# Kernel optimization log

Measured on AMD Instinct MI355X. Metric: run time of the kernel, lower is better.

Reference implementation:

```python
import jax, jax.numpy as jnp
import numpy as np

NOISE_WEIGHT = 1.0
CHAMFER_WEIGHT = 0.1
CHUNK = 1024


def _min_dist_chunked(a, b):
    """For each point in a [B,N,3], squared distance to nearest point in b [B,M,3].
    Processed in chunks of CHUNK points of `a` to avoid materializing [B,N,M].
    Returns [B,N]."""
    B, N, _ = a.shape
    b_sq = jnp.sum(b * b, axis=-1)  # [B,M]
    nc = N // CHUNK
    a_chunks = jnp.moveaxis(a.reshape(B, nc, CHUNK, 3), 1, 0)  # [nc,B,CHUNK,3]

    def body(carry, a_c):
        a_sq = jnp.sum(a_c * a_c, axis=-1)  # [B,CHUNK]
        # d[b,i,j] = |a_i|^2 + |b_j|^2 - 2 a_i.b_j
        d = a_sq[:, :, None] + b_sq[:, None, :] - 2.0 * jnp.einsum('bid,bjd->bij', a_c, b)
        d = jnp.maximum(d, 0.0)
        return carry, jnp.min(d, axis=2)  # [B,CHUNK]

    _, mins = jax.lax.scan(body, None, a_chunks)  # [nc,B,CHUNK]
    return jnp.moveaxis(mins, 0, 1).reshape(B, N)


def chamfer_distance(pred, target):
    d_pt = _min_dist_chunked(pred, target)   # [B,N]
    d_tp = _min_dist_chunked(target, pred)   # [B,M]
    return jnp.mean(d_pt, axis=1) + jnp.mean(d_tp, axis=1)  # [B]


def setup_inputs() -> dict:
    key = jax.random.key(0)
    k1, k2, k3, k4 = jax.random.split(key, 4)
    B, N = 8, 16384
    return {
        'predicted_noise': jax.random.normal(k1, (B, N, 3), dtype=jnp.float32),
        'actual_noise': jax.random.normal(k2, (B, N, 3), dtype=jnp.float32),
        'predicted_points_coarse': jax.random.normal(k3, (B, N, 3), dtype=jnp.float32),
        'target_points_coarse': jax.random.normal(k4, (B, N, 3), dtype=jnp.float32),
    }


def reference(predicted_noise, actual_noise, predicted_points_coarse, target_points_coarse):
    noise_loss = jnp.mean(jnp.abs(predicted_noise - actual_noise))
    chamfer_loss = jnp.mean(chamfer_distance(predicted_points_coarse, target_points_coarse))
    total_loss = NOISE_WEIGHT * noise_loss + CHAMFER_WEIGHT * chamfer_loss
    return total_loss
```

## Files before the change

### kernel.cpp

```cpp
#include <hip/hip_runtime.h>
#include <stdint.h>

#define NPTS        16384
#define BATCH       8
#define JC          512
#define NCHUNK      (NPTS / JC)
#define QPB         128
#define QBLKS       (NPTS / QPB)
#define CHAM_BLOCKS (BATCH * 2 * QBLKS)
#define NOISE_N     (BATCH * NPTS * 3)
#define NOISE_V4    (NOISE_N / 4)
#define NOISE_BLOCKS (NOISE_V4 / 256)
#define NPTS_TOT    (BATCH * NPTS)

#define WS_NOISE_PART 0
#define WS_CHAM_PART  4096
#define WS_PK_PRED    16384
#define WS_PK_TARG    (WS_PK_PRED + 8 * NPTS_TOT)
#define WS_R_PRED     (WS_PK_TARG + 8 * NPTS_TOT)
#define WS_R_TARG     (WS_R_PRED + 4 * NPTS_TOT)

using halfx8 = __attribute__((ext_vector_type(8))) _Float16;
using f32x16 = __attribute__((ext_vector_type(16))) float;

__device__ __forceinline__ unsigned short f2h(float f) {
  union { _Float16 h; unsigned short s; } v; v.h = (_Float16)f; return v.s;
}
__device__ __forceinline__ float h2f(unsigned short s) {
  union { _Float16 h; unsigned short u; } v; v.u = s; return (float)v.h;
}

__global__ void pack_kernel(const float* __restrict__ pred,
                            const float* __restrict__ targ,
                            ushort4* __restrict__ pk_pred,
                            ushort4* __restrict__ pk_targ,
                            float* __restrict__ r_pred,
                            float* __restrict__ r_targ) {
  int i = blockIdx.x * 256 + threadIdx.x;
  if (i >= NPTS_TOT) return;
  {
    float x = pred[3*i+0], y = pred[3*i+1], z = pred[3*i+2];
    float s = __builtin_fmaf(x, x, __builtin_fmaf(y, y, z*z));
    pk_pred[i] = make_ushort4(f2h(x), f2h(y), f2h(z), f2h(s));
    r_pred[i] = s;
  }
  {
    float x = targ[3*i+0], y = targ[3*i+1], z = targ[3*i+2];
    float s = __builtin_fmaf(x, x, __builtin_fmaf(y, y, z*z));
    pk_targ[i] = make_ushort4(f2h(x), f2h(y), f2h(z), f2h(s));
    r_targ[i] = s;
  }
}

__global__ void noise_kernel(const float4* __restrict__ a,
                             const float4* __restrict__ b,
                             float* __restrict__ part) {
  int i = blockIdx.x * 256 + threadIdx.x;
  float4 pa = a[i], pb = b[i];
  float s = fabsf(pa.x-pb.x) + fabsf(pa.y-pb.y) + fabsf(pa.z-pb.z) + fabsf(pa.w-pb.w);
  for (int o = 1; o < 64; o <<= 1) s += __shfl_xor(s, o);
  __shared__ float ws4[4];
  int lane = threadIdx.x & 63, wv = threadIdx.x >> 6;
  if (lane == 0) ws4[wv] = s;
  __syncthreads();
  if (threadIdx.x == 0) part[blockIdx.x] = ws4[0] + ws4[1] + ws4[2] + ws4[3];
}

__global__ __launch_bounds__(256, 4)
void chamfer_kernel(const ushort4* __restrict__ pk_pred,
                    const ushort4* __restrict__ pk_targ,
                    const float* __restrict__ r_pred,
                    const float* __restrict__ r_targ,
                    float* __restrict__ part) {
  __shared__ __align__(16) ushort4 buf[2][JC];
  __shared__ float wsum[4];

  const int tid  = threadIdx.x;
  const int lane = tid & 63;
  const int wv   = tid >> 6;
  const int col  = lane & 31;

  const int blk  = blockIdx.x;
  const int qblk = blk & (QBLKS - 1);
  const int bd   = blk >> 7;
  const int dir  = bd & 1;
  const int b    = bd >> 1;

  const ushort4* qpk = dir ? pk_targ : pk_pred;
  const float*   qr  = dir ? r_targ  : r_pred;
  const ushort4* ref = dir ? pk_pred : pk_targ;
  qpk += b * NPTS; qr += b * NPTS; ref += b * NPTS;

  union { halfx8 v; unsigned int u[4]; } fb;
  fb.u[0] = 0; fb.u[1] = 0; fb.u[2] = 0; fb.u[3] = 0;
  const int q = qblk * QPB + wv * 32 + col;
  if (lane < 32) {
    ushort4 t = qpk[q];
    unsigned short nx = f2h(-2.f * h2f(t.x));
    unsigned short ny = f2h(-2.f * h2f(t.y));
    unsigned short nz = f2h(-2.f * h2f(t.z));
    fb.u[0] = ((unsigned)ny << 16) | nx;
    fb.u[1] = (0x3C00u << 16) | nz;
  }

  f32x16 czero = {0.f,0.f,0.f,0.f, 0.f,0.f,0.f,0.f, 0.f,0.f,0.f,0.f, 0.f,0.f,0.f,0.f};

  union { halfx8 v; unsigned int u[4]; } fa;
  fa.u[2] = 0; fa.u[3] = 0;

  auto stage = [&](int c, int pb) {
    const char* g = (const char*)ref + (size_t)c * (JC * 8) + wv * 1024 + lane * 16;
    char* l = (char*)&buf[pb][wv * 128];
    __builtin_amdgcn_global_load_lds(
        (const __attribute__((address_space(1))) unsigned int*)(uintptr_t)g,
        (__attribute__((address_space(3))) unsigned int*)(unsigned int)(uintptr_t)l,
        16, 0, 0);
  };

  stage(0, 0);

  float m = 1e30f;
  for (int c = 0; c < NCHUNK; ++c) {
    const int pp = c & 1;
    __syncthreads();
    if (c + 1 < NCHUNK) stage(c + 1, pp ^ 1);
    const uint2* lp = (const uint2*)&buf[pp][col];
#pragma unroll
    for (int t = 0; t < 16; ++t) {
      uint2 av = lp[t * 32];
      fa.u[0] = av.x; fa.u[1] = av.y;
      f32x16 d = __builtin_amdgcn_mfma_f32_32x32x16_f16(fa.v, fb.v, czero, 0, 0, 0);
      float t0 = fminf(fminf(d[0],  d[1]),  d[2]);
      float t1 = fminf(fminf(d[3],  d[4]),  d[5]);
      float t2 = fminf(fminf(d[6],  d[7]),  d[8]);
      float t3 = fminf(fminf(d[9],  d[10]), d[11]);
      float t4 = fminf(fminf(d[12], d[13]), d[14]);
      t0 = fminf(fminf(t0, t1), t2);
      t3 = fminf(fminf(t3, t4), d[15]);
      m  = fminf(fminf(m, t0), t3);
    }
  }

  m = fminf(m, __shfl_xor(m, 32));
  float rq = qr[q];
  float dmin = fmaxf(rq + m, 0.f);
  float v = (lane < 32) ? dmin : 0.f;
  for (int o = 1; o < 32; o <<= 1) v += __shfl_xor(v, o);
  if (lane == 0) wsum[wv] = v;
  __syncthreads();
  if (tid == 0) part[blockIdx.x] = wsum[0] + wsum[1] + wsum[2] + wsum[3];
}

__global__ void final_kernel(const float* __restrict__ part_noise,
                             const float* __restrict__ part_cham,
                             float* __restrict__ out) {
  __shared__ float red[256];
  float s = 0.f;
  for (int i = threadIdx.x; i < NOISE_BLOCKS; i += 256) s += part_noise[i];
  float t = 0.f;
  for (int i = threadIdx.x; i < CHAM_BLOCKS; i += 256) t += part_cham[i];
  red[threadIdx.x] = s; __syncthreads();
  for (int o = 128; o; o >>= 1) { if (threadIdx.x < o) red[threadIdx.x] += red[threadIdx.x + o]; __syncthreads(); }
  float noise_sum = red[0];
  __syncthreads();
  red[threadIdx.x] = t; __syncthreads();
  for (int o = 128; o; o >>= 1) { if (threadIdx.x < o) red[threadIdx.x] += red[threadIdx.x + o]; __syncthreads(); }
  if (threadIdx.x == 0)
    out[0] = noise_sum * (1.f / NOISE_N) + 0.1f * red[0] * (1.f / NPTS_TOT);
}

extern "C" void kernel_launch(void* const* d_in, const int* in_sizes, int n_in,
                              void* d_out, int out_size, void* d_ws, size_t ws_size,
                              hipStream_t stream) {
  const float* pn = (const float*)d_in[0];
  const float* an = (const float*)d_in[1];
  const float* pp = (const float*)d_in[2];
  const float* tp = (const float*)d_in[3];

  char* ws = (char*)d_ws;
  float*   noise_part = (float*)(ws + WS_NOISE_PART);
  float*   cham_part  = (float*)(ws + WS_CHAM_PART);
  ushort4* pk_pred    = (ushort4*)(ws + WS_PK_PRED);
  ushort4* pk_targ    = (ushort4*)(ws + WS_PK_TARG);
  float*   r_pred     = (float*)(ws + WS_R_PRED);
  float*   r_targ     = (float*)(ws + WS_R_TARG);

  pack_kernel<<<NPTS_TOT / 256, 256, 0, stream>>>(pp, tp, pk_pred, pk_targ, r_pred, r_targ);
  noise_kernel<<<NOISE_BLOCKS, 256, 0, stream>>>((const float4*)pn, (const float4*)an, noise_part);
  chamfer_kernel<<<CHAM_BLOCKS, 256, 0, stream>>>(pk_pred, pk_targ, r_pred, r_targ, cham_part);
  final_kernel<<<1, 256, 0, stream>>>(noise_part, cham_part, (float*)d_out);
}
```

Before: 180.4 us.

## Load 16-byte A fragments covering four reference points and fuse noise into pack

```diff
diff --git a/kernel.cpp b/kernel.cpp
--- a/kernel.cpp
+++ b/kernel.cpp
@@ -10,8 +10,8 @@
 #define CHAM_BLOCKS (BATCH * 2 * QBLKS)
 #define NOISE_N     (BATCH * NPTS * 3)
 #define NOISE_V4    (NOISE_N / 4)
-#define NOISE_BLOCKS (NOISE_V4 / 256)
 #define NPTS_TOT    (BATCH * NPTS)
+#define PACK_BLOCKS (NPTS_TOT / 256)
 
 #define WS_NOISE_PART 0
 #define WS_CHAM_PART  4096
@@ -22,46 +22,51 @@
 
 using halfx8 = __attribute__((ext_vector_type(8))) _Float16;
 using f32x16 = __attribute__((ext_vector_type(16))) float;
-
-__device__ __forceinline__ unsigned short f2h(float f) {
+using intx4  = __attribute__((ext_vector_type(4))) int;
+
+__device__ __forceinline__ unsigned int f2h(float f) {
   union { _Float16 h; unsigned short s; } v; v.h = (_Float16)f; return v.s;
 }
 __device__ __forceinline__ float h2f(unsigned short s) {
   union { _Float16 h; unsigned short u; } v; v.u = s; return (float)v.h;
 }
-
-__global__ void pack_kernel(const float* __restrict__ pred,
-                            const float* __restrict__ targ,
-                            ushort4* __restrict__ pk_pred,
-                            ushort4* __restrict__ pk_targ,
-                            float* __restrict__ r_pred,
-                            float* __restrict__ r_targ) {
+__device__ __forceinline__ float min3(float a, float b, float c) {
+  return fminf(fminf(a, b), c);
+}
+
+__global__ void pack_noise_kernel(const float* __restrict__ pred,
+                                  const float* __restrict__ targ,
+                                  const float4* __restrict__ na,
+                                  const float4* __restrict__ nb,
+                                  ushort4* __restrict__ pk_pred,
+                                  ushort4* __restrict__ pk_targ,
+                                  float* __restrict__ r_pred,
+                                  float* __restrict__ r_targ,
+                                  float* __restrict__ part) {
   int i = blockIdx.x * 256 + threadIdx.x;
-  if (i >= NPTS_TOT) return;
   {
     float x = pred[3*i+0], y = pred[3*i+1], z = pred[3*i+2];
     float s = __builtin_fmaf(x, x, __builtin_fmaf(y, y, z*z));
-    pk_pred[i] = make_ushort4(f2h(x), f2h(y), f2h(z), f2h(s));
+    pk_pred[i] = make_ushort4((unsigned short)f2h(x), (unsigned short)f2h(y),
+                              (unsigned short)f2h(z), (unsigned short)f2h(s));
     r_pred[i] = s;
   }
   {
     float x = targ[3*i+0], y = targ[3*i+1], z = targ[3*i+2];
     float s = __builtin_fmaf(x, x, __builtin_fmaf(y, y, z*z));
-    pk_targ[i] = make_ushort4(f2h(x), f2h(y), f2h(z), f2h(s));
+    pk_targ[i] = make_ushort4((unsigned short)f2h(x), (unsigned short)f2h(y),
+                              (unsigned short)f2h(z), (unsigned short)f2h(s));
     r_targ[i] = s;
   }
-}
-
-__global__ void noise_kernel(const float4* __restrict__ a,
-                             const float4* __restrict__ b,
-                             float* __restrict__ part) {
-  int i = blockIdx.x * 256 + threadIdx.x;
-  float4 pa = a[i], pb = b[i];
-  float s = fabsf(pa.x-pb.x) + fabsf(pa.y-pb.y) + fabsf(pa.z-pb.z) + fabsf(pa.w-pb.w);
-  for (int o = 1; o < 64; o <<= 1) s += __shfl_xor(s, o);
+  float sn = 0.f;
+  if (i < NOISE_V4) {
+    float4 pa = na[i], pb = nb[i];
+    sn = fabsf(pa.x-pb.x) + fabsf(pa.y-pb.y) + fabsf(pa.z-pb.z) + fabsf(pa.w-pb.w);
+  }
+  for (int o = 1; o < 64; o <<= 1) sn += __shfl_xor(sn, o);
   __shared__ float ws4[4];
   int lane = threadIdx.x & 63, wv = threadIdx.x >> 6;
-  if (lane == 0) ws4[wv] = s;
+  if (lane == 0) ws4[wv] = sn;
   __syncthreads();
   if (threadIdx.x == 0) part[blockIdx.x] = ws4[0] + ws4[1] + ws4[2] + ws4[3];
 }
@@ -91,22 +96,23 @@
   const ushort4* ref = dir ? pk_pred : pk_targ;
   qpk += b * NPTS; qr += b * NPTS; ref += b * NPTS;
 
-  union { halfx8 v; unsigned int u[4]; } fb;
-  fb.u[0] = 0; fb.u[1] = 0; fb.u[2] = 0; fb.u[3] = 0;
   const int q = qblk * QPB + wv * 32 + col;
-  if (lane < 32) {
-    ushort4 t = qpk[q];
-    unsigned short nx = f2h(-2.f * h2f(t.x));
-    unsigned short ny = f2h(-2.f * h2f(t.y));
-    unsigned short nz = f2h(-2.f * h2f(t.z));
-    fb.u[0] = ((unsigned)ny << 16) | nx;
-    fb.u[1] = (0x3C00u << 16) | nz;
-  }
+  ushort4 qt = qpk[q];
+  unsigned int nx = f2h(-2.f * h2f(qt.x));
+  unsigned int ny = f2h(-2.f * h2f(qt.y));
+  unsigned int nz = f2h(-2.f * h2f(qt.z));
+  unsigned int lo = (ny << 16) | nx;
+  unsigned int hi = (0x3C00u << 16) | nz;
+  const bool hh = (lane >= 32);
+
+  union BF { halfx8 v; unsigned int u[4]; };
+  BF fb0, fb1, fb2, fb3;
+  fb0.u[0] = hh ? 0u : lo; fb0.u[1] = hh ? 0u : hi; fb0.u[2] = 0u;           fb0.u[3] = 0u;
+  fb1.u[0] = 0u;           fb1.u[1] = 0u;           fb1.u[2] = hh ? 0u : lo; fb1.u[3] = hh ? 0u : hi;
+  fb2.u[0] = hh ? lo : 0u; fb2.u[1] = hh ? hi : 0u; fb2.u[2] = 0u;           fb2.u[3] = 0u;
+  fb3.u[0] = 0u;           fb3.u[1] = 0u;           fb3.u[2] = hh ? lo : 0u; fb3.u[3] = hh ? hi : 0u;
 
   f32x16 czero = {0.f,0.f,0.f,0.f, 0.f,0.f,0.f,0.f, 0.f,0.f,0.f,0.f, 0.f,0.f,0.f,0.f};
-
-  union { halfx8 v; unsigned int u[4]; } fa;
-  fa.u[2] = 0; fa.u[3] = 0;
 
   auto stage = [&](int c, int pb) {
     const char* g = (const char*)ref + (size_t)c * (JC * 8) + wv * 1024 + lane * 16;
@@ -119,25 +125,34 @@
 
   stage(0, 0);
 
+  union AF { intx4 i; halfx8 h; };
+
   float m = 1e30f;
   for (int c = 0; c < NCHUNK; ++c) {
     const int pp = c & 1;
     __syncthreads();
     if (c + 1 < NCHUNK) stage(c + 1, pp ^ 1);
-    const uint2* lp = (const uint2*)&buf[pp][col];
+    const char* base = (const char*)&buf[pp][0];
 #pragma unroll
-    for (int t = 0; t < 16; ++t) {
-      uint2 av = lp[t * 32];
-      fa.u[0] = av.x; fa.u[1] = av.y;
-      f32x16 d = __builtin_amdgcn_mfma_f32_32x32x16_f16(fa.v, fb.v, czero, 0, 0, 0);
-      float t0 = fminf(fminf(d[0],  d[1]),  d[2]);
-      float t1 = fminf(fminf(d[3],  d[4]),  d[5]);
-      float t2 = fminf(fminf(d[6],  d[7]),  d[8]);
-      float t3 = fminf(fminf(d[9],  d[10]), d[11]);
-      float t4 = fminf(fminf(d[12], d[13]), d[14]);
-      t0 = fminf(fminf(t0, t1), t2);
-      t3 = fminf(fminf(t3, t4), d[15]);
-      m  = fminf(fminf(m, t0), t3);
+    for (int t = 0; t < 4; ++t) {
+      AF fa;
+      fa.i = *(const intx4*)(base + t * 1024 + lane * 16);
+      f32x16 d0 = __builtin_amdgcn_mfma_f32_32x32x16_f16(fa.h, fb0.v, czero, 0, 0, 0);
+      f32x16 d1 = __builtin_amdgcn_mfma_f32_32x32x16_f16(fa.h, fb1.v, czero, 0, 0, 0);
+      f32x16 d2 = __builtin_amdgcn_mfma_f32_32x32x16_f16(fa.h, fb2.v, czero, 0, 0, 0);
+      f32x16 d3 = __builtin_amdgcn_mfma_f32_32x32x16_f16(fa.h, fb3.v, czero, 0, 0, 0);
+#pragma unroll
+      for (int r = 0; r < 4; ++r) {
+        const f32x16& d = (r == 0) ? d0 : (r == 1) ? d1 : (r == 2) ? d2 : d3;
+        float t0 = min3(d[0],  d[1],  d[2]);
+        float t1 = min3(d[3],  d[4],  d[5]);
+        float t2 = min3(d[6],  d[7],  d[8]);
+        float t3 = min3(d[9],  d[10], d[11]);
+        float t4 = min3(d[12], d[13], d[14]);
+        float u0 = min3(t0, t1, t2);
+        float u1 = min3(t3, t4, d[15]);
+        m = min3(m, u0, u1);
+      }
     }
   }
 
@@ -156,7 +171,7 @@
                              float* __restrict__ out) {
   __shared__ float red[256];
   float s = 0.f;
-  for (int i = threadIdx.x; i < NOISE_BLOCKS; i += 256) s += part_noise[i];
+  for (int i = threadIdx.x; i < PACK_BLOCKS; i += 256) s += part_noise[i];
   float t = 0.f;
   for (int i = threadIdx.x; i < CHAM_BLOCKS; i += 256) t += part_cham[i];
   red[threadIdx.x] = s; __syncthreads();
@@ -185,8 +200,8 @@
   float*   r_pred     = (float*)(ws + WS_R_PRED);
   float*   r_targ     = (float*)(ws + WS_R_TARG);
 
-  pack_kernel<<<NPTS_TOT / 256, 256, 0, stream>>>(pp, tp, pk_pred, pk_targ, r_pred, r_targ);
-  noise_kernel<<<NOISE_BLOCKS, 256, 0, stream>>>((const float4*)pn, (const float4*)an, noise_part);
+  pack_noise_kernel<<<PACK_BLOCKS, 256, 0, stream>>>(pp, tp, (const float4*)pn, (const float4*)an,
+                                                     pk_pred, pk_targ, r_pred, r_targ, noise_part);
   chamfer_kernel<<<CHAM_BLOCKS, 256, 0, stream>>>(pk_pred, pk_targ, r_pred, r_targ, cham_part);
   final_kernel<<<1, 256, 0, stream>>>(noise_part, cham_part, (float*)d_out);
 }
```

Result: faster. 170.7 us (-5.4%).
